# Optimization experiments

Hardware: AMD Instinct MI355X
Metric: run time of the kernel (lower is better)

Reference implementation:

```python
import jax, jax.numpy as jnp
import numpy as np

# Dims: batch=64, n_cols=512, n_e=80, n_i=20, embed=512
DT_OVER_TAU = 0.1  # leaky rate-neuron integration constant (dt/tau)

B, C, NE, NI, E = 64, 512, 80, 20, 512


def setup_inputs() -> dict:
    key = jax.random.key(0)
    ks = jax.random.split(key, 12)
    return {
        "thal": jax.random.normal(ks[0], (B, E), jnp.float32),
        "thal_increments": jax.random.normal(ks[1], (B, C, E), jnp.float32),
        "l23_fb": jax.random.normal(ks[2], (B, C, NE), jnp.float32),
        # state (rates nonnegative, membrane potentials gaussian)
        "r_e": jax.random.uniform(ks[3], (B, C, NE), jnp.float32),
        "r_i": jax.random.uniform(ks[4], (B, C, NI), jnp.float32),
        "e_v": jax.random.normal(ks[5], (B, C, NE), jnp.float32),
        "i_v": jax.random.normal(ks[6], (B, C, NI), jnp.float32),
        # learned params (per-column weight stacks)
        "input_proj": jax.random.normal(ks[7], (C, NE, E), jnp.float32) * (1.0 / np.sqrt(E).astype(np.float32)),
        "feedback_proj": jax.random.normal(ks[8], (C, NE, NE), jnp.float32) * (1.0 / np.sqrt(NE).astype(np.float32)),
        # static synapses: nonnegative weights, sign handled by E/I convention
        "W_ee": jax.random.uniform(ks[9], (C, NE, NE), jnp.float32) * (1.0 / np.sqrt(NE).astype(np.float32)),
        "W_ei": jax.random.uniform(ks[10], (C, NI, NE), jnp.float32) * (1.0 / np.sqrt(NE).astype(np.float32)),
        "W_ie": jax.random.uniform(ks[11], (C, NE, NI), jnp.float32) * (1.0 / np.sqrt(NI).astype(np.float32)),
    }


def reference(thal, thal_increments, l23_fb, r_e, r_i, e_v, i_v,
              input_proj, feedback_proj, W_ee, W_ei, W_ie):
    # thal [B,E] broadcast over columns + per-column increments -> [B,C,E]
    thal_full = thal[:, None, :] + thal_increments
    # external + feedback drive onto excitatory pop: [B,C,NE]
    I_ext = jnp.einsum('bce,coe->bco', thal_full, input_proj)
    I_fb = jnp.einsum('bce,coe->bco', l23_fb, feedback_proj)
    # synapse currents (static weights; E->E, E->I excitatory, I->E inhibitory)
    I_ee = jnp.einsum('bcp,cop->bco', r_e, W_ee)   # [B,C,NE]
    I_ei = jnp.einsum('bcp,cop->bco', r_e, W_ei)   # [B,C,NI]
    I_ie = -jnp.einsum('bcp,cop->bco', r_i, W_ie)  # [B,C,NE], inhibitory
    I_e_total = I_ext + I_fb + I_ee + I_ie
    I_i_total = I_ei
    # leaky rate-neuron state update: v <- v + dt/tau * (-v + I); r = relu(v)
    v_e_new = e_v + DT_OVER_TAU * (I_e_total - e_v)
    v_i_new = i_v + DT_OVER_TAU * (I_i_total - i_v)
    r_e_new = jax.nn.relu(v_e_new)
    r_i_new = jax.nn.relu(v_i_new)
    # (layer_outputs e_out/l23_out/l5_out all alias r_e_new; return new state too)
    return r_e_new, r_i_new, v_e_new, v_i_new
```

## Files before the change

### kernel.cpp

```cpp
#include <hip/hip_runtime.h>
#include <hip/hip_bf16.h>

typedef __attribute__((ext_vector_type(8))) short bf16x8;
typedef __attribute__((ext_vector_type(4))) float f32x4;
typedef unsigned short u16;

__device__ __forceinline__ u16 f2bf(float f) {
  __hip_bfloat16 h = __float2bfloat16(f);
  u16 u;
  __builtin_memcpy(&u, &h, 2);
  return u;
}
__device__ __forceinline__ void cvt4_store(u16* dst, float4 v) {
  u16 rr[4] = {f2bf(v.x), f2bf(v.y), f2bf(v.z), f2bf(v.w)};
  uint2 p;
  __builtin_memcpy(&p, rr, 8);
  *(uint2*)dst = p;
}
__device__ __forceinline__ bf16x8 pack8(float4 a, float4 b) {
  u16 h[8] = {f2bf(a.x), f2bf(a.y), f2bf(a.z), f2bf(a.w),
              f2bf(b.x), f2bf(b.y), f2bf(b.z), f2bf(b.w)};
  bf16x8 r;
  __builtin_memcpy(&r, h, 16);
  return r;
}


__global__ __launch_bounds__(512, 4) void ei_cols_mfma(
    const float* __restrict__ thal,
    const float* __restrict__ inc,
    const float* __restrict__ l23,
    const float* __restrict__ re_in,
    const float* __restrict__ ri_in,
    const float* __restrict__ ev_in,
    const float* __restrict__ iv_in,
    const float* __restrict__ in_proj,
    const float* __restrict__ fb_proj,
    const float* __restrict__ w_ee,
    const float* __restrict__ w_ei,
    const float* __restrict__ w_ie,
    float* __restrict__ out)
{
  __shared__ __align__(16) unsigned char smem[31744];
  const int c = blockIdx.x;
  const int tid = threadIdx.x;
  const int lane = tid & 63;
  const int wave = tid >> 6;
  const int nidx = lane & 15;
  const int quad = lane >> 4;
  const int mw = wave & 3;
  const int jh = wave >> 2;
  const int m0 = mw * 16;

  f32x4 acc_e[3], acc_i[2];
#pragma unroll
  for (int j = 0; j < 3; ++j) acc_e[j] = (f32x4){0.f, 0.f, 0.f, 0.f};
#pragma unroll
  for (int j = 0; j < 2; ++j) acc_i[j] = (f32x4){0.f, 0.f, 0.f, 0.f};

  const float* wA = in_proj + (size_t)c * 40960;

  float4 tv0[2], gv0[2], tv1[2], gv1[2];
  float4 fbv[3];

  auto loadA = [&](float4* tv, float4* gv, int k0) {
#pragma unroll
    for (int j = 0; j < 2; ++j) {
      int l = tid + j * 512;
      int b = l >> 4, kk = (l & 15) << 2;
      tv[j] = *(const float4*)(thal + b * 512 + k0 + kk);
      gv[j] = *(const float4*)(inc + (size_t)b * 262144 + (size_t)c * 512 + k0 + kk);
    }
  };
  auto storeA = [&](int p, float4* tv, float4* gv) {
    u16* A = (u16*)(smem + p * 9216);
#pragma unroll
    for (int j = 0; j < 2; ++j) {
      int l = tid + j * 512;
      int b = l >> 4, kk = (l & 15) << 2;
      float4 s;
      s.x = tv[j].x + gv[j].x; s.y = tv[j].y + gv[j].y;
      s.z = tv[j].z + gv[j].z; s.w = tv[j].w + gv[j].w;
      cvt4_store(A + b * 72 + kk, s);
    }
  };

  loadA(tv0, gv0, 0);
  storeA(0, tv0, gv0);
  loadA(tv1, gv1, 64);
  loadA(tv0, gv0, 128);

  for (int i = 0; i < 8; ++i) {
    __syncthreads();
    const int p1 = (i + 1) & 1;
    if (i < 7) {
      if (p1) storeA(1, tv1, gv1); else storeA(0, tv0, gv0);
    }
    if (i < 5) {
      if (p1) loadA(tv1, gv1, (i + 3) * 64); else loadA(tv0, gv0, (i + 3) * 64);
    }
    if (i == 5) {
#pragma unroll
      for (int j = 0; j < 3; ++j) {
        int l = tid + j * 512;
        if (l < 1280) {
          int b = l / 20, kk = (l % 20) << 2;
          fbv[j] = *(const float4*)(l23 + ((size_t)b * 512 + c) * 80 + kk);
        }
      }
    }
    if (i == 7) {
      u16* As = (u16*)(smem + 18432);
#pragma unroll
      for (int j = 0; j < 3; ++j) {
        int l = tid + j * 512;
        if (l < 1280) {
          int b = l / 20, kk = (l % 20) << 2;
          cvt4_store(As + b * 104 + kk, fbv[j]);
        }
      }
      if (tid < 128) {
        int b = tid >> 1, off = 80 + (tid & 1) * 8;
        *(uint4*)(As + b * 104 + off) = (uint4){0u, 0u, 0u, 0u};
      }
    }
    const u16* A = (const u16*)(smem + (i & 1) * 9216);
    const float* wb = wA + i * 64;
#pragma unroll
    for (int kk0 = 0; kk0 < 64; kk0 += 32) {
      bf16x8 a = *(const bf16x8*)(A + (m0 + nidx) * 72 + kk0 + quad * 8);
      if (jh == 0) {
#pragma unroll
        for (int j = 0; j < 3; ++j) {
          const float* p = wb + (size_t)(j * 16 + nidx) * 512 + kk0 + quad * 8;
          bf16x8 b = pack8(*(const float4*)p, *(const float4*)(p + 4));
          acc_e[j] = __builtin_amdgcn_mfma_f32_16x16x32_bf16(a, b, acc_e[j], 0, 0, 0);
        }
      } else {
#pragma unroll
        for (int j = 0; j < 2; ++j) {
          const float* p = wb + (size_t)((3 + j) * 16 + nidx) * 512 + kk0 + quad * 8;
          bf16x8 b = pack8(*(const float4*)p, *(const float4*)(p + 4));
          acc_e[j] = __builtin_amdgcn_mfma_f32_16x16x32_bf16(a, b, acc_e[j], 0, 0, 0);
        }
      }
    }
  }

  float4 rev[3];
#pragma unroll
  for (int j = 0; j < 3; ++j) {
    int l = tid + j * 512;
    if (l < 1280) {
      int b = l / 20, kk = (l % 20) << 2;
      rev[j] = *(const float4*)(re_in + ((size_t)b * 512 + c) * 80 + kk);
    }
  }
  __syncthreads();
  {
    const u16* As = (const u16*)(smem + 18432);
    const float* fb = fb_proj + (size_t)c * 6400;
#pragma unroll
    for (int kk0 = 0; kk0 < 96; kk0 += 32) {
      bf16x8 a = *(const bf16x8*)(As + (m0 + nidx) * 104 + kk0 + quad * 8);
      const bool full = (kk0 < 64) || (quad < 2);
      if (jh == 0) {
#pragma unroll
        for (int j = 0; j < 3; ++j) {
          const float* p = fb + (size_t)(j * 16 + nidx) * 80 + kk0 + quad * 8;
          float4 w0 = {0.f, 0.f, 0.f, 0.f}, w1 = {0.f, 0.f, 0.f, 0.f};
          if (full) { w0 = *(const float4*)p; w1 = *(const float4*)(p + 4); }
          bf16x8 b = pack8(w0, w1);
          acc_e[j] = __builtin_amdgcn_mfma_f32_16x16x32_bf16(a, b, acc_e[j], 0, 0, 0);
        }
      } else {
#pragma unroll
        for (int j = 0; j < 2; ++j) {
          const float* p = fb + (size_t)((3 + j) * 16 + nidx) * 80 + kk0 + quad * 8;
          float4 w0 = {0.f, 0.f, 0.f, 0.f}, w1 = {0.f, 0.f, 0.f, 0.f};
          if (full) { w0 = *(const float4*)p; w1 = *(const float4*)(p + 4); }
          bf16x8 b = pack8(w0, w1);
          acc_e[j] = __builtin_amdgcn_mfma_f32_16x16x32_bf16(a, b, acc_e[j], 0, 0, 0);
        }
      }
    }
  }

  __syncthreads();
  {
    u16* Asw = (u16*)(smem + 18432);
#pragma unroll
    for (int j = 0; j < 3; ++j) {
      int l = tid + j * 512;
      if (l < 1280) {
        int b = l / 20, kk = (l % 20) << 2;
        cvt4_store(Asw + b * 104 + kk, rev[j]);
      }
    }
    if (tid < 128) {
      int b = tid >> 1, off = 80 + (tid & 1) * 8;
      *(uint4*)(Asw + b * 104 + off) = (uint4){0u, 0u, 0u, 0u};
    }
  }
  float4 riv;
  if (tid < 320) {
    int b = tid / 5, kk = (tid % 5) << 2;
    riv = *(const float4*)(ri_in + ((size_t)b * 512 + c) * 20 + kk);
  }
  __syncthreads();
  {
    const u16* As = (const u16*)(smem + 18432);
    const float* wee = w_ee + (size_t)c * 6400;
    const float* wei = w_ei + (size_t)c * 1600;
#pragma unroll
    for (int kk0 = 0; kk0 < 96; kk0 += 32) {
      bf16x8 a = *(const bf16x8*)(As + (m0 + nidx) * 104 + kk0 + quad * 8);
      const bool full = (kk0 < 64) || (quad < 2);
      if (jh == 0) {
#pragma unroll
        for (int j = 0; j < 3; ++j) {
          const float* p = wee + (size_t)(j * 16 + nidx) * 80 + kk0 + quad * 8;
          float4 w0 = {0.f, 0.f, 0.f, 0.f}, w1 = {0.f, 0.f, 0.f, 0.f};
          if (full) { w0 = *(const float4*)p; w1 = *(const float4*)(p + 4); }
          bf16x8 b = pack8(w0, w1);
          acc_e[j] = __builtin_amdgcn_mfma_f32_16x16x32_bf16(a, b, acc_e[j], 0, 0, 0);
        }
      } else {
#pragma unroll
        for (int j = 0; j < 2; ++j) {
          const float* p = wee + (size_t)((3 + j) * 16 + nidx) * 80 + kk0 + quad * 8;
          float4 w0 = {0.f, 0.f, 0.f, 0.f}, w1 = {0.f, 0.f, 0.f, 0.f};
          if (full) { w0 = *(const float4*)p; w1 = *(const float4*)(p + 4); }
          bf16x8 b = pack8(w0, w1);
          acc_e[j] = __builtin_amdgcn_mfma_f32_16x16x32_bf16(a, b, acc_e[j], 0, 0, 0);
        }
#pragma unroll
        for (int j = 0; j < 2; ++j) {
          int row = j * 16 + nidx;
          float4 w0 = {0.f, 0.f, 0.f, 0.f}, w1 = {0.f, 0.f, 0.f, 0.f};
          if (row < 20 && full) {
            const float* p = wei + (size_t)row * 80 + kk0 + quad * 8;
            w0 = *(const float4*)p; w1 = *(const float4*)(p + 4);
          }
          bf16x8 b = pack8(w0, w1);
          acc_i[j] = __builtin_amdgcn_mfma_f32_16x16x32_bf16(a, b, acc_i[j], 0, 0, 0);
        }
      }
    }
  }

  __syncthreads();
  {
    u16* Ri = (u16*)(smem + 18432);
    if (tid < 320) {
      int b = tid / 5, kk = (tid % 5) << 2;
      cvt4_store(Ri + b * 40 + kk, riv);
    }
    if (tid < 192) {
      int b = tid / 3, kk = 20 + (tid % 3) * 4;
      *(uint2*)(Ri + b * 40 + kk) = (uint2){0u, 0u};
    }
  }
  float evr[3][4], ivr[2][4];
  const int row0 = m0 + quad * 4;
  if (jh == 0) {
#pragma unroll
    for (int j = 0; j < 3; ++j) {
      int col = j * 16 + nidx;
#pragma unroll
      for (int r = 0; r < 4; ++r)
        evr[j][r] = ev_in[((size_t)(row0 + r) * 512 + c) * 80 + col];
    }
  } else {
#pragma unroll
    for (int j = 0; j < 2; ++j) {
      int col = 48 + j * 16 + nidx;
#pragma unroll
      for (int r = 0; r < 4; ++r)
        evr[j][r] = ev_in[((size_t)(row0 + r) * 512 + c) * 80 + col];
    }
#pragma unroll
    for (int j = 0; j < 2; ++j) {
      int col = j * 16 + nidx;
#pragma unroll
      for (int r = 0; r < 4; ++r)
        ivr[j][r] = (col < 20)
            ? iv_in[((size_t)(row0 + r) * 512 + c) * 20 + col] : 0.f;
    }
  }
  __syncthreads();
  {
    const u16* Ri = (const u16*)(smem + 18432);
    bf16x8 a = *(const bf16x8*)(Ri + (m0 + nidx) * 40 + quad * 8);
    auto wieF = [&](int row) -> bf16x8 {
      const float* p = w_ie + (size_t)c * 1600 + row * 20 + quad * 8;
      float4 w0 = {0.f, 0.f, 0.f, 0.f}, w1 = {0.f, 0.f, 0.f, 0.f};
      if (quad < 2) { w0 = *(const float4*)p; w1 = *(const float4*)(p + 4); }
      else if (quad == 2) { w0 = *(const float4*)p; }
      w0.x = -w0.x; w0.y = -w0.y; w0.z = -w0.z; w0.w = -w0.w;
      w1.x = -w1.x; w1.y = -w1.y; w1.z = -w1.z; w1.w = -w1.w;
      return pack8(w0, w1);
    };
    if (jh == 0) {
#pragma unroll
      for (int j = 0; j < 3; ++j) {
        bf16x8 b = wieF(j * 16 + nidx);
        acc_e[j] = __builtin_amdgcn_mfma_f32_16x16x32_bf16(a, b, acc_e[j], 0, 0, 0);
      }
    } else {
#pragma unroll
      for (int j = 0; j < 2; ++j) {
        bf16x8 b = wieF((3 + j) * 16 + nidx);
        acc_e[j] = __builtin_amdgcn_mfma_f32_16x16x32_bf16(a, b, acc_e[j], 0, 0, 0);
      }
    }
  }

  {
    const size_t R_ri = 2621440u;
    const size_t R_ve = 3276800u;
    const size_t R_vi = 5898240u;
    if (jh == 0) {
#pragma unroll
      for (int j = 0; j < 3; ++j) {
        int col = j * 16 + nidx;
#pragma unroll
        for (int r = 0; r < 4; ++r) {
          size_t g = ((size_t)(row0 + r) * 512 + c) * 80 + col;
          float e0 = evr[j][r];
          float v = e0 + 0.1f * (acc_e[j][r] - e0);
          out[g] = fmaxf(v, 0.f);
          out[R_ve + g] = v;
        }
      }
    } else {
#pragma unroll
      for (int j = 0; j < 2; ++j) {
        int col = 48 + j * 16 + nidx;
#pragma unroll
        for (int r = 0; r < 4; ++r) {
          size_t g = ((size_t)(row0 + r) * 512 + c) * 80 + col;
          float e0 = evr[j][r];
          float v = e0 + 0.1f * (acc_e[j][r] - e0);
          out[g] = fmaxf(v, 0.f);
          out[R_ve + g] = v;
        }
      }
#pragma unroll
      for (int j = 0; j < 2; ++j) {
        int col = j * 16 + nidx;
        if (col < 20) {
#pragma unroll
          for (int r = 0; r < 4; ++r) {
            size_t g = ((size_t)(row0 + r) * 512 + c) * 20 + col;
            float i0 = ivr[j][r];
            float v = i0 + 0.1f * (acc_i[j][r] - i0);
            out[R_ri + g] = fmaxf(v, 0.f);
            out[R_vi + g] = v;
          }
        }
      }
    }
  }
}

extern "C" void kernel_launch(void* const* d_in, const int* in_sizes, int n_in,
                              void* d_out, int out_size, void* d_ws, size_t ws_size,
                              hipStream_t stream) {
  const float* thal = (const float*)d_in[0];
  const float* inc = (const float*)d_in[1];
  const float* l23 = (const float*)d_in[2];
  const float* re = (const float*)d_in[3];
  const float* ri = (const float*)d_in[4];
  const float* ev = (const float*)d_in[5];
  const float* iv = (const float*)d_in[6];
  const float* in_proj = (const float*)d_in[7];
  const float* fb_proj = (const float*)d_in[8];
  const float* w_ee = (const float*)d_in[9];
  const float* w_ei = (const float*)d_in[10];
  const float* w_ie = (const float*)d_in[11];
  float* out = (float*)d_out;
  ei_cols_mfma<<<dim3(512), dim3(512), 0, stream>>>(
      thal, inc, l23, re, ri, ev, iv, in_proj, fb_proj, w_ee, w_ei, w_ie, out);
}
```

Baseline: 259.2 us.

## Load MFMA A-operands directly from global memory, dropping shared-memory staging and barriers

Each wave now reads its own A-fragment rows (thal+increment, l23, r_e, r_i) straight from global memory into registers and converts them to bf16 there. This replaces the cooperative shared-memory staging and the block-wide __syncthreads between stages. The input-projection loop is restructured as a register double-buffered prefetch over K in 32-wide steps. The cost is that each A row is now loaded separately by both wave halves (jh=0/1), doubling A-operand global traffic, with less coalesced per-lane 32-byte accesses and more register pressure.

```diff
diff --git a/kernel.cpp b/kernel.cpp
--- a/kernel.cpp
+++ b/kernel.cpp
@@ -10,12 +10,6 @@
   u16 u;
   __builtin_memcpy(&u, &h, 2);
   return u;
-}
-__device__ __forceinline__ void cvt4_store(u16* dst, float4 v) {
-  u16 rr[4] = {f2bf(v.x), f2bf(v.y), f2bf(v.z), f2bf(v.w)};
-  uint2 p;
-  __builtin_memcpy(&p, rr, 8);
-  *(uint2*)dst = p;
 }
 __device__ __forceinline__ bf16x8 pack8(float4 a, float4 b) {
   u16 h[8] = {f2bf(a.x), f2bf(a.y), f2bf(a.z), f2bf(a.w),
@@ -41,7 +35,6 @@
     const float* __restrict__ w_ie,
     float* __restrict__ out)
 {
-  __shared__ __align__(16) unsigned char smem[31744];
   const int c = blockIdx.x;
   const int tid = threadIdx.x;
   const int lane = tid & 63;
@@ -51,6 +44,8 @@
   const int mw = wave & 3;
   const int jh = wave >> 2;
   const int m0 = mw * 16;
+  const int brow = m0 + nidx;
+  const int q8 = quad * 8;
 
   f32x4 acc_e[3], acc_i[2];
 #pragma unroll
@@ -58,242 +53,214 @@
 #pragma unroll
   for (int j = 0; j < 2; ++j) acc_i[j] = (f32x4){0.f, 0.f, 0.f, 0.f};
 
+  const float* incR = inc + (size_t)brow * 262144 + (size_t)c * 512;
+  const float* thalR = thal + (size_t)brow * 512;
   const float* wA = in_proj + (size_t)c * 40960;
 
-  float4 tv0[2], gv0[2], tv1[2], gv1[2];
-  float4 fbv[3];
-
-  auto loadA = [&](float4* tv, float4* gv, int k0) {
+  if (jh == 0) {
+    float4 ca0 = *(const float4*)(incR + q8);
+    float4 ca1 = *(const float4*)(incR + q8 + 4);
+    float4 ct0 = *(const float4*)(thalR + q8);
+    float4 ct1 = *(const float4*)(thalR + q8 + 4);
+    float4 cw[3][2];
+#pragma unroll
+    for (int j = 0; j < 3; ++j) {
+      const float* p = wA + (size_t)(j * 16 + nidx) * 512 + q8;
+      cw[j][0] = *(const float4*)p;
+      cw[j][1] = *(const float4*)(p + 4);
+    }
+    for (int k0 = 0; k0 < 480; k0 += 32) {
+      const int kn = k0 + 32 + q8;
+      float4 na0 = *(const float4*)(incR + kn);
+      float4 na1 = *(const float4*)(incR + kn + 4);
+      float4 nt0 = *(const float4*)(thalR + kn);
+      float4 nt1 = *(const float4*)(thalR + kn + 4);
+      float4 nw[3][2];
+#pragma unroll
+      for (int j = 0; j < 3; ++j) {
+        const float* p = wA + (size_t)(j * 16 + nidx) * 512 + kn;
+        nw[j][0] = *(const float4*)p;
+        nw[j][1] = *(const float4*)(p + 4);
+      }
+      float4 s0, s1;
+      s0.x = ca0.x + ct0.x; s0.y = ca0.y + ct0.y;
+      s0.z = ca0.z + ct0.z; s0.w = ca0.w + ct0.w;
+      s1.x = ca1.x + ct1.x; s1.y = ca1.y + ct1.y;
+      s1.z = ca1.z + ct1.z; s1.w = ca1.w + ct1.w;
+      bf16x8 af = pack8(s0, s1);
+#pragma unroll
+      for (int j = 0; j < 3; ++j) {
+        bf16x8 bf = pack8(cw[j][0], cw[j][1]);
+        acc_e[j] = __builtin_amdgcn_mfma_f32_16x16x32_bf16(af, bf, acc_e[j], 0, 0, 0);
+      }
+      ca0 = na0; ca1 = na1; ct0 = nt0; ct1 = nt1;
+#pragma unroll
+      for (int j = 0; j < 3; ++j) { cw[j][0] = nw[j][0]; cw[j][1] = nw[j][1]; }
+    }
+    {
+      float4 s0, s1;
+      s0.x = ca0.x + ct0.x; s0.y = ca0.y + ct0.y;
+      s0.z = ca0.z + ct0.z; s0.w = ca0.w + ct0.w;
+      s1.x = ca1.x + ct1.x; s1.y = ca1.y + ct1.y;
+      s1.z = ca1.z + ct1.z; s1.w = ca1.w + ct1.w;
+      bf16x8 af = pack8(s0, s1);
+#pragma unroll
+      for (int j = 0; j < 3; ++j) {
+        bf16x8 bf = pack8(cw[j][0], cw[j][1]);
+        acc_e[j] = __builtin_amdgcn_mfma_f32_16x16x32_bf16(af, bf, acc_e[j], 0, 0, 0);
+      }
+    }
+  } else {
+    float4 ca0 = *(const float4*)(incR + q8);
+    float4 ca1 = *(const float4*)(incR + q8 + 4);
+    float4 ct0 = *(const float4*)(thalR + q8);
+    float4 ct1 = *(const float4*)(thalR + q8 + 4);
+    float4 cw[2][2];
 #pragma unroll
     for (int j = 0; j < 2; ++j) {
-      int l = tid + j * 512;
-      int b = l >> 4, kk = (l & 15) << 2;
-      tv[j] = *(const float4*)(thal + b * 512 + k0 + kk);
-      gv[j] = *(const float4*)(inc + (size_t)b * 262144 + (size_t)c * 512 + k0 + kk);
-    }
-  };
-  auto storeA = [&](int p, float4* tv, float4* gv) {
-    u16* A = (u16*)(smem + p * 9216);
-#pragma unroll
-    for (int j = 0; j < 2; ++j) {
-      int l = tid + j * 512;
-      int b = l >> 4, kk = (l & 15) << 2;
-      float4 s;
-      s.x = tv[j].x + gv[j].x; s.y = tv[j].y + gv[j].y;
-      s.z = tv[j].z + gv[j].z; s.w = tv[j].w + gv[j].w;
-      cvt4_store(A + b * 72 + kk, s);
-    }
-  };
-
-  loadA(tv0, gv0, 0);
-  storeA(0, tv0, gv0);
-  loadA(tv1, gv1, 64);
-  loadA(tv0, gv0, 128);
-
-  for (int i = 0; i < 8; ++i) {
-    __syncthreads();
-    const int p1 = (i + 1) & 1;
-    if (i < 7) {
-      if (p1) storeA(1, tv1, gv1); else storeA(0, tv0, gv0);
-    }
-    if (i < 5) {
-      if (p1) loadA(tv1, gv1, (i + 3) * 64); else loadA(tv0, gv0, (i + 3) * 64);
-    }
-    if (i == 5) {
-#pragma unroll
-      for (int j = 0; j < 3; ++j) {
-        int l = tid + j * 512;
-        if (l < 1280) {
-          int b = l / 20, kk = (l % 20) << 2;
-          fbv[j] = *(const float4*)(l23 + ((size_t)b * 512 + c) * 80 + kk);
-        }
-      }
-    }
-    if (i == 7) {
-      u16* As = (u16*)(smem + 18432);
-#pragma unroll
-      for (int j = 0; j < 3; ++j) {
-        int l = tid + j * 512;
-        if (l < 1280) {
-          int b = l / 20, kk = (l % 20) << 2;
-          cvt4_store(As + b * 104 + kk, fbv[j]);
-        }
-      }
-      if (tid < 128) {
-        int b = tid >> 1, off = 80 + (tid & 1) * 8;
-        *(uint4*)(As + b * 104 + off) = (uint4){0u, 0u, 0u, 0u};
-      }
-    }
-    const u16* A = (const u16*)(smem + (i & 1) * 9216);
-    const float* wb = wA + i * 64;
-#pragma unroll
-    for (int kk0 = 0; kk0 < 64; kk0 += 32) {
-      bf16x8 a = *(const bf16x8*)(A + (m0 + nidx) * 72 + kk0 + quad * 8);
+      const float* p = wA + (size_t)((3 + j) * 16 + nidx) * 512 + q8;
+      cw[j][0] = *(const float4*)p;
+      cw[j][1] = *(const float4*)(p + 4);
+    }
+    for (int k0 = 0; k0 < 480; k0 += 32) {
+      const int kn = k0 + 32 + q8;
+      float4 na0 = *(const float4*)(incR + kn);
+      float4 na1 = *(const float4*)(incR + kn + 4);
+      float4 nt0 = *(const float4*)(thalR + kn);
+      float4 nt1 = *(const float4*)(thalR + kn + 4);
+      float4 nw[2][2];
+#pragma unroll
+      for (int j = 0; j < 2; ++j) {
+        const float* p = wA + (size_t)((3 + j) * 16 + nidx) * 512 + kn;
+        nw[j][0] = *(const float4*)p;
+        nw[j][1] = *(const float4*)(p + 4);
+      }
+      float4 s0, s1;
+      s0.x = ca0.x + ct0.x; s0.y = ca0.y + ct0.y;
+      s0.z = ca0.z + ct0.z; s0.w = ca0.w + ct0.w;
+      s1.x = ca1.x + ct1.x; s1.y = ca1.y + ct1.y;
+      s1.z = ca1.z + ct1.z; s1.w = ca1.w + ct1.w;
+      bf16x8 af = pack8(s0, s1);
+#pragma unroll
+      for (int j = 0; j < 2; ++j) {
+        bf16x8 bf = pack8(cw[j][0], cw[j][1]);
+        acc_e[j] = __builtin_amdgcn_mfma_f32_16x16x32_bf16(af, bf, acc_e[j], 0, 0, 0);
+      }
+      ca0 = na0; ca1 = na1; ct0 = nt0; ct1 = nt1;
+#pragma unroll
+      for (int j = 0; j < 2; ++j) { cw[j][0] = nw[j][0]; cw[j][1] = nw[j][1]; }
+    }
+    {
+      float4 s0, s1;
+      s0.x = ca0.x + ct0.x; s0.y = ca0.y + ct0.y;
+      s0.z = ca0.z + ct0.z; s0.w = ca0.w + ct0.w;
+      s1.x = ca1.x + ct1.x; s1.y = ca1.y + ct1.y;
+      s1.z = ca1.z + ct1.z; s1.w = ca1.w + ct1.w;
+      bf16x8 af = pack8(s0, s1);
+#pragma unroll
+      for (int j = 0; j < 2; ++j) {
+        bf16x8 bf = pack8(cw[j][0], cw[j][1]);
+        acc_e[j] = __builtin_amdgcn_mfma_f32_16x16x32_bf16(af, bf, acc_e[j], 0, 0, 0);
+      }
+    }
+  }
+
+  {
+    const float* l23R = l23 + ((size_t)brow * 512 + c) * 80;
+    const float* fb = fb_proj + (size_t)c * 6400;
+#pragma unroll
+    for (int kk0 = 0; kk0 < 96; kk0 += 32) {
+      const bool full = (kk0 < 64) || (quad < 2);
+      float4 a0 = {0.f, 0.f, 0.f, 0.f}, a1 = {0.f, 0.f, 0.f, 0.f};
+      if (full) {
+        a0 = *(const float4*)(l23R + kk0 + q8);
+        a1 = *(const float4*)(l23R + kk0 + q8 + 4);
+      }
+      bf16x8 af = pack8(a0, a1);
       if (jh == 0) {
 #pragma unroll
         for (int j = 0; j < 3; ++j) {
-          const float* p = wb + (size_t)(j * 16 + nidx) * 512 + kk0 + quad * 8;
-          bf16x8 b = pack8(*(const float4*)p, *(const float4*)(p + 4));
-          acc_e[j] = __builtin_amdgcn_mfma_f32_16x16x32_bf16(a, b, acc_e[j], 0, 0, 0);
+          float4 w0 = {0.f, 0.f, 0.f, 0.f}, w1 = {0.f, 0.f, 0.f, 0.f};
+          if (full) {
+            const float* p = fb + (size_t)(j * 16 + nidx) * 80 + kk0 + q8;
+            w0 = *(const float4*)p; w1 = *(const float4*)(p + 4);
+          }
+          bf16x8 bf = pack8(w0, w1);
+          acc_e[j] = __builtin_amdgcn_mfma_f32_16x16x32_bf16(af, bf, acc_e[j], 0, 0, 0);
         }
       } else {
 #pragma unroll
         for (int j = 0; j < 2; ++j) {
-          const float* p = wb + (size_t)((3 + j) * 16 + nidx) * 512 + kk0 + quad * 8;
-          bf16x8 b = pack8(*(const float4*)p, *(const float4*)(p + 4));
-          acc_e[j] = __builtin_amdgcn_mfma_f32_16x16x32_bf16(a, b, acc_e[j], 0, 0, 0);
-        }
-      }
-    }
-  }
-
-  float4 rev[3];
-#pragma unroll
-  for (int j = 0; j < 3; ++j) {
-    int l = tid + j * 512;
-    if (l < 1280) {
-      int b = l / 20, kk = (l % 20) << 2;
-      rev[j] = *(const float4*)(re_in + ((size_t)b * 512 + c) * 80 + kk);
-    }
-  }
-  __syncthreads();
+          float4 w0 = {0.f, 0.f, 0.f, 0.f}, w1 = {0.f, 0.f, 0.f, 0.f};
+          if (full) {
+            const float* p = fb + (size_t)((3 + j) * 16 + nidx) * 80 + kk0 + q8;
+            w0 = *(const float4*)p; w1 = *(const float4*)(p + 4);
+          }
+          bf16x8 bf = pack8(w0, w1);
+          acc_e[j] = __builtin_amdgcn_mfma_f32_16x16x32_bf16(af, bf, acc_e[j], 0, 0, 0);
+        }
+      }
+    }
+  }
+
   {
-    const u16* As = (const u16*)(smem + 18432);
-    const float* fb = fb_proj + (size_t)c * 6400;
-#pragma unroll
-    for (int kk0 = 0; kk0 < 96; kk0 += 32) {
-      bf16x8 a = *(const bf16x8*)(As + (m0 + nidx) * 104 + kk0 + quad * 8);
-      const bool full = (kk0 < 64) || (quad < 2);
-      if (jh == 0) {
-#pragma unroll
-        for (int j = 0; j < 3; ++j) {
-          const float* p = fb + (size_t)(j * 16 + nidx) * 80 + kk0 + quad * 8;
-          float4 w0 = {0.f, 0.f, 0.f, 0.f}, w1 = {0.f, 0.f, 0.f, 0.f};
-          if (full) { w0 = *(const float4*)p; w1 = *(const float4*)(p + 4); }
-          bf16x8 b = pack8(w0, w1);
-          acc_e[j] = __builtin_amdgcn_mfma_f32_16x16x32_bf16(a, b, acc_e[j], 0, 0, 0);
-        }
-      } else {
-#pragma unroll
-        for (int j = 0; j < 2; ++j) {
-          const float* p = fb + (size_t)((3 + j) * 16 + nidx) * 80 + kk0 + quad * 8;
-          float4 w0 = {0.f, 0.f, 0.f, 0.f}, w1 = {0.f, 0.f, 0.f, 0.f};
-          if (full) { w0 = *(const float4*)p; w1 = *(const float4*)(p + 4); }
-          bf16x8 b = pack8(w0, w1);
-          acc_e[j] = __builtin_amdgcn_mfma_f32_16x16x32_bf16(a, b, acc_e[j], 0, 0, 0);
-        }
-      }
-    }
-  }
-
-  __syncthreads();
-  {
-    u16* Asw = (u16*)(smem + 18432);
-#pragma unroll
-    for (int j = 0; j < 3; ++j) {
-      int l = tid + j * 512;
-      if (l < 1280) {
-        int b = l / 20, kk = (l % 20) << 2;
-        cvt4_store(Asw + b * 104 + kk, rev[j]);
-      }
-    }
-    if (tid < 128) {
-      int b = tid >> 1, off = 80 + (tid & 1) * 8;
-      *(uint4*)(Asw + b * 104 + off) = (uint4){0u, 0u, 0u, 0u};
-    }
-  }
-  float4 riv;
-  if (tid < 320) {
-    int b = tid / 5, kk = (tid % 5) << 2;
-    riv = *(const float4*)(ri_in + ((size_t)b * 512 + c) * 20 + kk);
-  }
-  __syncthreads();
-  {
-    const u16* As = (const u16*)(smem + 18432);
+    const float* reR = re_in + ((size_t)brow * 512 + c) * 80;
     const float* wee = w_ee + (size_t)c * 6400;
     const float* wei = w_ei + (size_t)c * 1600;
 #pragma unroll
     for (int kk0 = 0; kk0 < 96; kk0 += 32) {
-      bf16x8 a = *(const bf16x8*)(As + (m0 + nidx) * 104 + kk0 + quad * 8);
       const bool full = (kk0 < 64) || (quad < 2);
+      float4 a0 = {0.f, 0.f, 0.f, 0.f}, a1 = {0.f, 0.f, 0.f, 0.f};
+      if (full) {
+        a0 = *(const float4*)(reR + kk0 + q8);
+        a1 = *(const float4*)(reR + kk0 + q8 + 4);
+      }
+      bf16x8 af = pack8(a0, a1);
       if (jh == 0) {
 #pragma unroll
         for (int j = 0; j < 3; ++j) {
-          const float* p = wee + (size_t)(j * 16 + nidx) * 80 + kk0 + quad * 8;
-          float4 w0 = {0.f, 0.f, 0.f, 0.f}, w1 = {0.f, 0.f, 0.f, 0.f};
-          if (full) { w0 = *(const float4*)p; w1 = *(const float4*)(p + 4); }
-          bf16x8 b = pack8(w0, w1);
-          acc_e[j] = __builtin_amdgcn_mfma_f32_16x16x32_bf16(a, b, acc_e[j], 0, 0, 0);
+          float4 w0 = {0.f, 0.f, 0.f, 0.f}, w1 = {0.f, 0.f, 0.f, 0.f};
+          if (full) {
+            const float* p = wee + (size_t)(j * 16 + nidx) * 80 + kk0 + q8;
+            w0 = *(const float4*)p; w1 = *(const float4*)(p + 4);
+          }
+          bf16x8 bf = pack8(w0, w1);
+          acc_e[j] = __builtin_amdgcn_mfma_f32_16x16x32_bf16(af, bf, acc_e[j], 0, 0, 0);
         }
       } else {
 #pragma unroll
         for (int j = 0; j < 2; ++j) {
-          const float* p = wee + (size_t)((3 + j) * 16 + nidx) * 80 + kk0 + quad * 8;
-          float4 w0 = {0.f, 0.f, 0.f, 0.f}, w1 = {0.f, 0.f, 0.f, 0.f};
-          if (full) { w0 = *(const float4*)p; w1 = *(const float4*)(p + 4); }
-          bf16x8 b = pack8(w0, w1);
-          acc_e[j] = __builtin_amdgcn_mfma_f32_16x16x32_bf16(a, b, acc_e[j], 0, 0, 0);
+          float4 w0 = {0.f, 0.f, 0.f, 0.f}, w1 = {0.f, 0.f, 0.f, 0.f};
+          if (full) {
+            const float* p = wee + (size_t)((3 + j) * 16 + nidx) * 80 + kk0 + q8;
+            w0 = *(const float4*)p; w1 = *(const float4*)(p + 4);
+          }
+          bf16x8 bf = pack8(w0, w1);
+          acc_e[j] = __builtin_amdgcn_mfma_f32_16x16x32_bf16(af, bf, acc_e[j], 0, 0, 0);
         }
 #pragma unroll
         for (int j = 0; j < 2; ++j) {
-          int row = j * 16 + nidx;
+          const int row = j * 16 + nidx;
           float4 w0 = {0.f, 0.f, 0.f, 0.f}, w1 = {0.f, 0.f, 0.f, 0.f};
           if (row < 20 && full) {
-            const float* p = wei + (size_t)row * 80 + kk0 + quad * 8;
-            w0 = *(const float4*)p; w1 = *(const float4*)(p + 4);
-          }
-          bf16x8 b = pack8(w0, w1);
-          acc_i[j] = __builtin_amdgcn_mfma_f32_16x16x32_bf16(a, b, acc_i[j], 0, 0, 0);
-        }
-      }
-    }
-  }
-
-  __syncthreads();
+            const float* p = wei + (size_t)row * 80 + kk0 + q8;
+            w0 = *(const float4*)p; w1 = *(const float4*)(p + 4);
+          }
+          bf16x8 bf = pack8(w0, w1);
+          acc_i[j] = __builtin_amdgcn_mfma_f32_16x16x32_bf16(af, bf, acc_i[j], 0, 0, 0);
+        }
+      }
+    }
+  }
+
   {
-    u16* Ri = (u16*)(smem + 18432);
-    if (tid < 320) {
-      int b = tid / 5, kk = (tid % 5) << 2;
-      cvt4_store(Ri + b * 40 + kk, riv);
-    }
-    if (tid < 192) {
-      int b = tid / 3, kk = 20 + (tid % 3) * 4;
-      *(uint2*)(Ri + b * 40 + kk) = (uint2){0u, 0u};
-    }
-  }
-  float evr[3][4], ivr[2][4];
-  const int row0 = m0 + quad * 4;
-  if (jh == 0) {
-#pragma unroll
-    for (int j = 0; j < 3; ++j) {
-      int col = j * 16 + nidx;
-#pragma unroll
-      for (int r = 0; r < 4; ++r)
-        evr[j][r] = ev_in[((size_t)(row0 + r) * 512 + c) * 80 + col];
-    }
-  } else {
-#pragma unroll
-    for (int j = 0; j < 2; ++j) {
-      int col = 48 + j * 16 + nidx;
-#pragma unroll
-      for (int r = 0; r < 4; ++r)
-        evr[j][r] = ev_in[((size_t)(row0 + r) * 512 + c) * 80 + col];
-    }
-#pragma unroll
-    for (int j = 0; j < 2; ++j) {
-      int col = j * 16 + nidx;
-#pragma unroll
-      for (int r = 0; r < 4; ++r)
-        ivr[j][r] = (col < 20)
-            ? iv_in[((size_t)(row0 + r) * 512 + c) * 20 + col] : 0.f;
-    }
-  }
-  __syncthreads();
-  {
-    const u16* Ri = (const u16*)(smem + 18432);
-    bf16x8 a = *(const bf16x8*)(Ri + (m0 + nidx) * 40 + quad * 8);
+    const float* riR = ri_in + ((size_t)brow * 512 + c) * 20;
+    float4 a0 = {0.f, 0.f, 0.f, 0.f}, a1 = {0.f, 0.f, 0.f, 0.f};
+    if (quad <= 2) a0 = *(const float4*)(riR + q8);
+    if (quad <= 1) a1 = *(const float4*)(riR + q8 + 4);
+    bf16x8 af = pack8(a0, a1);
     auto wieF = [&](int row) -> bf16x8 {
-      const float* p = w_ie + (size_t)c * 1600 + row * 20 + quad * 8;
+      const float* p = w_ie + (size_t)c * 1600 + row * 20 + q8;
       float4 w0 = {0.f, 0.f, 0.f, 0.f}, w1 = {0.f, 0.f, 0.f, 0.f};
       if (quad < 2) { w0 = *(const float4*)p; w1 = *(const float4*)(p + 4); }
       else if (quad == 2) { w0 = *(const float4*)p; }
@@ -304,14 +271,14 @@
     if (jh == 0) {
 #pragma unroll
       for (int j = 0; j < 3; ++j) {
-        bf16x8 b = wieF(j * 16 + nidx);
-        acc_e[j] = __builtin_amdgcn_mfma_f32_16x16x32_bf16(a, b, acc_e[j], 0, 0, 0);
+        bf16x8 bf = wieF(j * 16 + nidx);
+        acc_e[j] = __builtin_amdgcn_mfma_f32_16x16x32_bf16(af, bf, acc_e[j], 0, 0, 0);
       }
     } else {
 #pragma unroll
       for (int j = 0; j < 2; ++j) {
-        bf16x8 b = wieF((3 + j) * 16 + nidx);
-        acc_e[j] = __builtin_amdgcn_mfma_f32_16x16x32_bf16(a, b, acc_e[j], 0, 0, 0);
+        bf16x8 bf = wieF((3 + j) * 16 + nidx);
+        acc_e[j] = __builtin_amdgcn_mfma_f32_16x16x32_bf16(af, bf, acc_e[j], 0, 0, 0);
       }
     }
   }
@@ -320,14 +287,15 @@
     const size_t R_ri = 2621440u;
     const size_t R_ve = 3276800u;
     const size_t R_vi = 5898240u;
+    const int row0 = m0 + quad * 4;
     if (jh == 0) {
 #pragma unroll
       for (int j = 0; j < 3; ++j) {
-        int col = j * 16 + nidx;
+        const int col = j * 16 + nidx;
 #pragma unroll
         for (int r = 0; r < 4; ++r) {
           size_t g = ((size_t)(row0 + r) * 512 + c) * 80 + col;
-          float e0 = evr[j][r];
+          float e0 = ev_in[g];
           float v = e0 + 0.1f * (acc_e[j][r] - e0);
           out[g] = fmaxf(v, 0.f);
           out[R_ve + g] = v;
@@ -336,11 +304,11 @@
     } else {
 #pragma unroll
       for (int j = 0; j < 2; ++j) {
-        int col = 48 + j * 16 + nidx;
+        const int col = 48 + j * 16 + nidx;
 #pragma unroll
         for (int r = 0; r < 4; ++r) {
           size_t g = ((size_t)(row0 + r) * 512 + c) * 80 + col;
-          float e0 = evr[j][r];
+          float e0 = ev_in[g];
           float v = e0 + 0.1f * (acc_e[j][r] - e0);
           out[g] = fmaxf(v, 0.f);
           out[R_ve + g] = v;
@@ -348,12 +316,12 @@
       }
 #pragma unroll
       for (int j = 0; j < 2; ++j) {
-        int col = j * 16 + nidx;
+        const int col = j * 16 + nidx;
         if (col < 20) {
 #pragma unroll
           for (int r = 0; r < 4; ++r) {
             size_t g = ((size_t)(row0 + r) * 512 + c) * 20 + col;
-            float i0 = ivr[j][r];
+            float i0 = iv_in[g];
             float v = i0 + 0.1f * (acc_i[j][r] - i0);
             out[R_ri + g] = fmaxf(v, 0.f);
             out[R_vi + g] = v;
```

After: 285.3 us. 10.1% more time.

## Split each column block into four smaller blocks over output half and batch half

Applied to the files above, without the earlier changes.

Replaces the single 512-thread block per column with a 512x2x2 grid of 128-thread blocks. Each block covers one output half (oh) and 32 batch rows, with shared memory cut to match. The A-tile pipeline becomes a simpler single-register-set scheme whose next-stage store happens after the MFMAs. The aim is more, smaller blocks for better occupancy and load balance, at the cost that each weight tile is now loaded by both batch-half blocks and the thal+increment sum is rebuilt by both output-half blocks.

```diff
diff --git a/kernel.cpp b/kernel.cpp
--- a/kernel.cpp
+++ b/kernel.cpp
@@ -26,7 +26,7 @@
 }
 
 
-__global__ __launch_bounds__(512, 4) void ei_cols_mfma(
+__global__ __launch_bounds__(128, 4) void ei_cols_mfma(
     const float* __restrict__ thal,
     const float* __restrict__ inc,
     const float* __restrict__ l23,
@@ -41,16 +41,17 @@
     const float* __restrict__ w_ie,
     float* __restrict__ out)
 {
-  __shared__ __align__(16) unsigned char smem[31744];
+  __shared__ __align__(16) unsigned char smem[18432];
   const int c = blockIdx.x;
+  const int oh = blockIdx.y;
+  const int bh32 = blockIdx.z * 32;
   const int tid = threadIdx.x;
   const int lane = tid & 63;
   const int wave = tid >> 6;
   const int nidx = lane & 15;
   const int quad = lane >> 4;
-  const int mw = wave & 3;
-  const int jh = wave >> 2;
-  const int m0 = mw * 16;
+  const int q8 = quad * 8;
+  const int lrow = wave * 16 + nidx;
 
   f32x4 acc_e[3], acc_i[2];
 #pragma unroll
@@ -60,23 +61,24 @@
 
   const float* wA = in_proj + (size_t)c * 40960;
 
-  float4 tv0[2], gv0[2], tv1[2], gv1[2];
-  float4 fbv[3];
-
-  auto loadA = [&](float4* tv, float4* gv, int k0) {
-#pragma unroll
-    for (int j = 0; j < 2; ++j) {
-      int l = tid + j * 512;
+  float4 tv[4], gv[4];
+  float4 fbv[5];
+
+  auto load_regs = [&](int k0) {
+#pragma unroll
+    for (int j = 0; j < 4; ++j) {
+      int l = tid + j * 128;
       int b = l >> 4, kk = (l & 15) << 2;
-      tv[j] = *(const float4*)(thal + b * 512 + k0 + kk);
-      gv[j] = *(const float4*)(inc + (size_t)b * 262144 + (size_t)c * 512 + k0 + kk);
+      tv[j] = *(const float4*)(thal + (bh32 + b) * 512 + k0 + kk);
+      gv[j] = *(const float4*)(inc + (size_t)(bh32 + b) * 262144 +
+                               (size_t)c * 512 + k0 + kk);
     }
   };
-  auto storeA = [&](int p, float4* tv, float4* gv) {
-    u16* A = (u16*)(smem + p * 9216);
-#pragma unroll
-    for (int j = 0; j < 2; ++j) {
-      int l = tid + j * 512;
+  auto store_buf = [&](int p) {
+    u16* A = (u16*)(smem + p * 4608);
+#pragma unroll
+    for (int j = 0; j < 4; ++j) {
+      int l = tid + j * 128;
       int b = l >> 4, kk = (l & 15) << 2;
       float4 s;
       s.x = tv[j].x + gv[j].x; s.y = tv[j].y + gv[j].y;
@@ -85,161 +87,151 @@
     }
   };
 
-  loadA(tv0, gv0, 0);
-  storeA(0, tv0, gv0);
-  loadA(tv1, gv1, 64);
-  loadA(tv0, gv0, 128);
-
+  load_regs(0);
+  store_buf(0);
   for (int i = 0; i < 8; ++i) {
     __syncthreads();
-    const int p1 = (i + 1) & 1;
-    if (i < 7) {
-      if (p1) storeA(1, tv1, gv1); else storeA(0, tv0, gv0);
-    }
-    if (i < 5) {
-      if (p1) loadA(tv1, gv1, (i + 3) * 64); else loadA(tv0, gv0, (i + 3) * 64);
-    }
+    if (i < 7) load_regs((i + 1) * 64);
     if (i == 5) {
 #pragma unroll
-      for (int j = 0; j < 3; ++j) {
-        int l = tid + j * 512;
-        if (l < 1280) {
-          int b = l / 20, kk = (l % 20) << 2;
-          fbv[j] = *(const float4*)(l23 + ((size_t)b * 512 + c) * 80 + kk);
-        }
+      for (int j = 0; j < 5; ++j) {
+        int l = tid + j * 128;
+        int b = l / 20, kk = (l % 20) << 2;
+        fbv[j] = *(const float4*)(l23 + ((size_t)(bh32 + b) * 512 + c) * 80 + kk);
       }
     }
     if (i == 7) {
-      u16* As = (u16*)(smem + 18432);
-#pragma unroll
-      for (int j = 0; j < 3; ++j) {
-        int l = tid + j * 512;
-        if (l < 1280) {
-          int b = l / 20, kk = (l % 20) << 2;
-          cvt4_store(As + b * 104 + kk, fbv[j]);
-        }
-      }
-      if (tid < 128) {
-        int b = tid >> 1, off = 80 + (tid & 1) * 8;
-        *(uint4*)(As + b * 104 + off) = (uint4){0u, 0u, 0u, 0u};
-      }
-    }
-    const u16* A = (const u16*)(smem + (i & 1) * 9216);
+      u16* As = (u16*)(smem + 9216);
+#pragma unroll
+      for (int j = 0; j < 5; ++j) {
+        int l = tid + j * 128;
+        int b = l / 20, kk = (l % 20) << 2;
+        cvt4_store(As + b * 104 + kk, fbv[j]);
+      }
+    }
+    const u16* A = (const u16*)(smem + (i & 1) * 4608);
     const float* wb = wA + i * 64;
 #pragma unroll
     for (int kk0 = 0; kk0 < 64; kk0 += 32) {
-      bf16x8 a = *(const bf16x8*)(A + (m0 + nidx) * 72 + kk0 + quad * 8);
-      if (jh == 0) {
+      bf16x8 a = *(const bf16x8*)(A + lrow * 72 + kk0 + q8);
+      if (oh == 0) {
 #pragma unroll
         for (int j = 0; j < 3; ++j) {
-          const float* p = wb + (size_t)(j * 16 + nidx) * 512 + kk0 + quad * 8;
+          const float* p = wb + (size_t)(j * 16 + nidx) * 512 + kk0 + q8;
           bf16x8 b = pack8(*(const float4*)p, *(const float4*)(p + 4));
           acc_e[j] = __builtin_amdgcn_mfma_f32_16x16x32_bf16(a, b, acc_e[j], 0, 0, 0);
         }
       } else {
 #pragma unroll
         for (int j = 0; j < 2; ++j) {
-          const float* p = wb + (size_t)((3 + j) * 16 + nidx) * 512 + kk0 + quad * 8;
+          const float* p = wb + (size_t)((3 + j) * 16 + nidx) * 512 + kk0 + q8;
           bf16x8 b = pack8(*(const float4*)p, *(const float4*)(p + 4));
           acc_e[j] = __builtin_amdgcn_mfma_f32_16x16x32_bf16(a, b, acc_e[j], 0, 0, 0);
         }
       }
     }
-  }
-
-  float4 rev[3];
-#pragma unroll
-  for (int j = 0; j < 3; ++j) {
-    int l = tid + j * 512;
-    if (l < 1280) {
+    if (i < 7) store_buf((i + 1) & 1);
+  }
+
+  float4 rev[5];
+#pragma unroll
+  for (int j = 0; j < 5; ++j) {
+    int l = tid + j * 128;
+    int b = l / 20, kk = (l % 20) << 2;
+    rev[j] = *(const float4*)(re_in + ((size_t)(bh32 + b) * 512 + c) * 80 + kk);
+  }
+  __syncthreads();
+  {
+    const u16* As = (const u16*)(smem + 9216);
+    const float* fb = fb_proj + (size_t)c * 6400;
+#pragma unroll
+    for (int kk0 = 0; kk0 < 96; kk0 += 32) {
+      const bool full = (kk0 < 64) || (quad < 2);
+      bf16x8 a = {0, 0, 0, 0, 0, 0, 0, 0};
+      if (full) a = *(const bf16x8*)(As + lrow * 104 + kk0 + q8);
+      if (oh == 0) {
+#pragma unroll
+        for (int j = 0; j < 3; ++j) {
+          float4 w0 = {0.f, 0.f, 0.f, 0.f}, w1 = {0.f, 0.f, 0.f, 0.f};
+          if (full) {
+            const float* p = fb + (size_t)(j * 16 + nidx) * 80 + kk0 + q8;
+            w0 = *(const float4*)p; w1 = *(const float4*)(p + 4);
+          }
+          bf16x8 b = pack8(w0, w1);
+          acc_e[j] = __builtin_amdgcn_mfma_f32_16x16x32_bf16(a, b, acc_e[j], 0, 0, 0);
+        }
+      } else {
+#pragma unroll
+        for (int j = 0; j < 2; ++j) {
+          float4 w0 = {0.f, 0.f, 0.f, 0.f}, w1 = {0.f, 0.f, 0.f, 0.f};
+          if (full) {
+            const float* p = fb + (size_t)((3 + j) * 16 + nidx) * 80 + kk0 + q8;
+            w0 = *(const float4*)p; w1 = *(const float4*)(p + 4);
+          }
+          bf16x8 b = pack8(w0, w1);
+          acc_e[j] = __builtin_amdgcn_mfma_f32_16x16x32_bf16(a, b, acc_e[j], 0, 0, 0);
+        }
+      }
+    }
+  }
+
+  __syncthreads();
+  {
+    u16* Asw = (u16*)(smem + 9216);
+#pragma unroll
+    for (int j = 0; j < 5; ++j) {
+      int l = tid + j * 128;
       int b = l / 20, kk = (l % 20) << 2;
-      rev[j] = *(const float4*)(re_in + ((size_t)b * 512 + c) * 80 + kk);
-    }
-  }
-  __syncthreads();
-  {
-    const u16* As = (const u16*)(smem + 18432);
-    const float* fb = fb_proj + (size_t)c * 6400;
-#pragma unroll
-    for (int kk0 = 0; kk0 < 96; kk0 += 32) {
-      bf16x8 a = *(const bf16x8*)(As + (m0 + nidx) * 104 + kk0 + quad * 8);
-      const bool full = (kk0 < 64) || (quad < 2);
-      if (jh == 0) {
-#pragma unroll
-        for (int j = 0; j < 3; ++j) {
-          const float* p = fb + (size_t)(j * 16 + nidx) * 80 + kk0 + quad * 8;
-          float4 w0 = {0.f, 0.f, 0.f, 0.f}, w1 = {0.f, 0.f, 0.f, 0.f};
-          if (full) { w0 = *(const float4*)p; w1 = *(const float4*)(p + 4); }
-          bf16x8 b = pack8(w0, w1);
-          acc_e[j] = __builtin_amdgcn_mfma_f32_16x16x32_bf16(a, b, acc_e[j], 0, 0, 0);
-        }
-      } else {
-#pragma unroll
-        for (int j = 0; j < 2; ++j) {
-          const float* p = fb + (size_t)((3 + j) * 16 + nidx) * 80 + kk0 + quad * 8;
-          float4 w0 = {0.f, 0.f, 0.f, 0.f}, w1 = {0.f, 0.f, 0.f, 0.f};
-          if (full) { w0 = *(const float4*)p; w1 = *(const float4*)(p + 4); }
-          bf16x8 b = pack8(w0, w1);
-          acc_e[j] = __builtin_amdgcn_mfma_f32_16x16x32_bf16(a, b, acc_e[j], 0, 0, 0);
-        }
-      }
-    }
-  }
-
-  __syncthreads();
-  {
-    u16* Asw = (u16*)(smem + 18432);
-#pragma unroll
-    for (int j = 0; j < 3; ++j) {
-      int l = tid + j * 512;
-      if (l < 1280) {
-        int b = l / 20, kk = (l % 20) << 2;
-        cvt4_store(Asw + b * 104 + kk, rev[j]);
-      }
-    }
-    if (tid < 128) {
-      int b = tid >> 1, off = 80 + (tid & 1) * 8;
-      *(uint4*)(Asw + b * 104 + off) = (uint4){0u, 0u, 0u, 0u};
-    }
-  }
-  float4 riv;
-  if (tid < 320) {
-    int b = tid / 5, kk = (tid % 5) << 2;
-    riv = *(const float4*)(ri_in + ((size_t)b * 512 + c) * 20 + kk);
-  }
-  __syncthreads();
-  {
-    const u16* As = (const u16*)(smem + 18432);
+      cvt4_store(Asw + b * 104 + kk, rev[j]);
+    }
+  }
+  float4 riv[2];
+#pragma unroll
+  for (int j = 0; j < 2; ++j) {
+    int l = tid + j * 128;
+    if (l < 160) {
+      int b = l / 5, kk = (l % 5) << 2;
+      riv[j] = *(const float4*)(ri_in + ((size_t)(bh32 + b) * 512 + c) * 20 + kk);
+    }
+  }
+  __syncthreads();
+  {
+    const u16* As = (const u16*)(smem + 9216);
     const float* wee = w_ee + (size_t)c * 6400;
     const float* wei = w_ei + (size_t)c * 1600;
 #pragma unroll
     for (int kk0 = 0; kk0 < 96; kk0 += 32) {
-      bf16x8 a = *(const bf16x8*)(As + (m0 + nidx) * 104 + kk0 + quad * 8);
       const bool full = (kk0 < 64) || (quad < 2);
-      if (jh == 0) {
+      bf16x8 a = {0, 0, 0, 0, 0, 0, 0, 0};
+      if (full) a = *(const bf16x8*)(As + lrow * 104 + kk0 + q8);
+      if (oh == 0) {
 #pragma unroll
         for (int j = 0; j < 3; ++j) {
-          const float* p = wee + (size_t)(j * 16 + nidx) * 80 + kk0 + quad * 8;
-          float4 w0 = {0.f, 0.f, 0.f, 0.f}, w1 = {0.f, 0.f, 0.f, 0.f};
-          if (full) { w0 = *(const float4*)p; w1 = *(const float4*)(p + 4); }
+          float4 w0 = {0.f, 0.f, 0.f, 0.f}, w1 = {0.f, 0.f, 0.f, 0.f};
+          if (full) {
+            const float* p = wee + (size_t)(j * 16 + nidx) * 80 + kk0 + q8;
+            w0 = *(const float4*)p; w1 = *(const float4*)(p + 4);
+          }
           bf16x8 b = pack8(w0, w1);
           acc_e[j] = __builtin_amdgcn_mfma_f32_16x16x32_bf16(a, b, acc_e[j], 0, 0, 0);
         }
       } else {
 #pragma unroll
         for (int j = 0; j < 2; ++j) {
-          const float* p = wee + (size_t)((3 + j) * 16 + nidx) * 80 + kk0 + quad * 8;
-          float4 w0 = {0.f, 0.f, 0.f, 0.f}, w1 = {0.f, 0.f, 0.f, 0.f};
-          if (full) { w0 = *(const float4*)p; w1 = *(const float4*)(p + 4); }
+          float4 w0 = {0.f, 0.f, 0.f, 0.f}, w1 = {0.f, 0.f, 0.f, 0.f};
+          if (full) {
+            const float* p = wee + (size_t)((3 + j) * 16 + nidx) * 80 + kk0 + q8;
+            w0 = *(const float4*)p; w1 = *(const float4*)(p + 4);
+          }
           bf16x8 b = pack8(w0, w1);
           acc_e[j] = __builtin_amdgcn_mfma_f32_16x16x32_bf16(a, b, acc_e[j], 0, 0, 0);
         }
 #pragma unroll
         for (int j = 0; j < 2; ++j) {
-          int row = j * 16 + nidx;
+          const int row = j * 16 + nidx;
           float4 w0 = {0.f, 0.f, 0.f, 0.f}, w1 = {0.f, 0.f, 0.f, 0.f};
           if (row < 20 && full) {
-            const float* p = wei + (size_t)row * 80 + kk0 + quad * 8;
+            const float* p = wei + (size_t)row * 80 + kk0 + q8;
             w0 = *(const float4*)p; w1 = *(const float4*)(p + 4);
           }
           bf16x8 b = pack8(w0, w1);
@@ -251,19 +243,27 @@
 
   __syncthreads();
   {
-    u16* Ri = (u16*)(smem + 18432);
-    if (tid < 320) {
-      int b = tid / 5, kk = (tid % 5) << 2;
-      cvt4_store(Ri + b * 40 + kk, riv);
-    }
-    if (tid < 192) {
-      int b = tid / 3, kk = 20 + (tid % 3) * 4;
-      *(uint2*)(Ri + b * 40 + kk) = (uint2){0u, 0u};
+    u16* Ri = (u16*)(smem + 15872);
+#pragma unroll
+    for (int j = 0; j < 2; ++j) {
+      int l = tid + j * 128;
+      if (l < 160) {
+        int b = l / 5, kk = (l % 5) << 2;
+        cvt4_store(Ri + b * 40 + kk, riv[j]);
+      }
+    }
+#pragma unroll
+    for (int j = 0; j < 2; ++j) {
+      int l = tid + j * 128;
+      if (l < 160) {
+        int b = l / 5, off = 20 + (l % 5) * 4;
+        *(uint2*)(Ri + b * 40 + off) = (uint2){0u, 0u};
+      }
     }
   }
   float evr[3][4], ivr[2][4];
-  const int row0 = m0 + quad * 4;
-  if (jh == 0) {
+  const int row0 = bh32 + wave * 16 + quad * 4;
+  if (oh == 0) {
 #pragma unroll
     for (int j = 0; j < 3; ++j) {
       int col = j * 16 + nidx;
@@ -290,10 +290,10 @@
   }
   __syncthreads();
   {
-    const u16* Ri = (const u16*)(smem + 18432);
-    bf16x8 a = *(const bf16x8*)(Ri + (m0 + nidx) * 40 + quad * 8);
+    const u16* Ri = (const u16*)(smem + 15872);
+    bf16x8 a = *(const bf16x8*)(Ri + lrow * 40 + q8);
     auto wieF = [&](int row) -> bf16x8 {
-      const float* p = w_ie + (size_t)c * 1600 + row * 20 + quad * 8;
+      const float* p = w_ie + (size_t)c * 1600 + row * 20 + q8;
       float4 w0 = {0.f, 0.f, 0.f, 0.f}, w1 = {0.f, 0.f, 0.f, 0.f};
       if (quad < 2) { w0 = *(const float4*)p; w1 = *(const float4*)(p + 4); }
       else if (quad == 2) { w0 = *(const float4*)p; }
@@ -301,7 +301,7 @@
       w1.x = -w1.x; w1.y = -w1.y; w1.z = -w1.z; w1.w = -w1.w;
       return pack8(w0, w1);
     };
-    if (jh == 0) {
+    if (oh == 0) {
 #pragma unroll
       for (int j = 0; j < 3; ++j) {
         bf16x8 b = wieF(j * 16 + nidx);
@@ -320,10 +320,10 @@
     const size_t R_ri = 2621440u;
     const size_t R_ve = 3276800u;
     const size_t R_vi = 5898240u;
-    if (jh == 0) {
+    if (oh == 0) {
 #pragma unroll
       for (int j = 0; j < 3; ++j) {
-        int col = j * 16 + nidx;
+        const int col = j * 16 + nidx;
 #pragma unroll
         for (int r = 0; r < 4; ++r) {
           size_t g = ((size_t)(row0 + r) * 512 + c) * 80 + col;
@@ -336,7 +336,7 @@
     } else {
 #pragma unroll
       for (int j = 0; j < 2; ++j) {
-        int col = 48 + j * 16 + nidx;
+        const int col = 48 + j * 16 + nidx;
 #pragma unroll
         for (int r = 0; r < 4; ++r) {
           size_t g = ((size_t)(row0 + r) * 512 + c) * 80 + col;
@@ -348,7 +348,7 @@
       }
 #pragma unroll
       for (int j = 0; j < 2; ++j) {
-        int col = j * 16 + nidx;
+        const int col = j * 16 + nidx;
         if (col < 20) {
 #pragma unroll
           for (int r = 0; r < 4; ++r) {
@@ -380,6 +380,6 @@
   const float* w_ei = (const float*)d_in[10];
   const float* w_ie = (const float*)d_in[11];
   float* out = (float*)d_out;
-  ei_cols_mfma<<<dim3(512), dim3(512), 0, stream>>>(
+  ei_cols_mfma<<<dim3(512, 2, 2), dim3(128), 0, stream>>>(
       thal, inc, l23, re, ri, ev, iv, in_proj, fb_proj, w_ee, w_ei, w_ie, out);
 }
```

Result: slower. 276.9 us (+6.8%).
